# Kernel tuning notes

Hardware: AMD Instinct MI355X
Metric: run time of the kernel (lower is better)

The kernel has to match this reference:

```python
import jax, jax.numpy as jnp
import numpy as np

D_MODEL = 1024
N_HEADS = 16
HEAD_DIM = D_MODEL // N_HEADS


def setup_inputs() -> dict:
    key = jax.random.key(0)
    ks = jax.random.split(key, 6)
    B, S = 2, 2048
    scale = 1.0 / np.sqrt(D_MODEL)
    x = jax.random.normal(ks[0], (B, S, D_MODEL), dtype=jnp.float32)
    Wq = jax.random.normal(ks[1], (D_MODEL, D_MODEL), dtype=jnp.float32) * scale
    Wk = jax.random.normal(ks[2], (D_MODEL, D_MODEL), dtype=jnp.float32) * scale
    Wv = jax.random.normal(ks[3], (D_MODEL, D_MODEL), dtype=jnp.float32) * scale
    Wo = jax.random.normal(ks[4], (D_MODEL, D_MODEL), dtype=jnp.float32) * scale
    bo = jax.random.normal(ks[5], (D_MODEL,), dtype=jnp.float32) * 0.02
    return {"x": x, "Wq": Wq, "Wk": Wk, "Wv": Wv, "Wo": Wo, "bo": bo}


def reference(x, Wq, Wk, Wv, Wo, bo):
    B, S, _ = x.shape
    H, hd = N_HEADS, HEAD_DIM
    # qkv projections (no bias, qkv_bias=False)
    q = (x @ Wq).reshape(B, S, H, hd).transpose(0, 2, 1, 3)  # [B,H,S,hd]
    k = (x @ Wk).reshape(B, S, H, hd).transpose(0, 2, 1, 3)
    v = (x @ Wv).reshape(B, S, H, hd).transpose(0, 2, 1, 3)
    scores = jnp.einsum('bhqd,bhkd->bhqk', q, k)  # [B,H,S,S]
    causal = jnp.tril(jnp.ones((S, S), dtype=bool))  # True = keep
    scores = jnp.where(causal, scores, -jnp.inf)
    weights = jax.nn.softmax(scores / np.sqrt(hd), axis=-1)
    # dropout p=0.0 -> identity
    ctx = jnp.einsum('bhqk,bhkd->bhqd', weights, v)  # [B,H,S,hd]
    ctx = ctx.transpose(0, 2, 1, 3).reshape(B, S, H * hd)
    return ctx @ Wo + bo
```

## Files before the change

### kernel.cpp

```cpp
#include <hip/hip_runtime.h>
#include <hip/hip_bf16.h>
#include <stdint.h>

#define SEQ    2048
#define BATCH  2
#define DMODEL 1024
#define NHEADS 16
#define HDIM   64
#define MROWS  (BATCH*SEQ)

typedef __attribute__((ext_vector_type(8))) short bf16x8;
typedef __attribute__((ext_vector_type(4))) float f32x4;

__device__ inline void global_to_lds16(const void* g, void* l) {
  __builtin_amdgcn_global_load_lds(
      (const __attribute__((address_space(1))) uint32_t*)g,
      (__attribute__((address_space(3))) uint32_t*)l, 16, 0, 0);
}

__device__ inline unsigned short f2bf_bits(float f) {
  __hip_bfloat16 h = __float2bfloat16(f);
  return *(unsigned short*)&h;
}

__global__ void cvt_x(const float* __restrict__ x, __hip_bfloat16* __restrict__ xb) {
  int i = (blockIdx.x * 256 + threadIdx.x) * 4;
  float4 v = *(const float4*)(x + i);
  ushort4 o;
  o.x = f2bf_bits(v.x); o.y = f2bf_bits(v.y);
  o.z = f2bf_bits(v.z); o.w = f2bf_bits(v.w);
  *(ushort4*)(xb + i) = o;
}

__global__ void trans_w(const float* __restrict__ Wq, const float* __restrict__ Wk,
                        const float* __restrict__ Wv, const float* __restrict__ Wo,
                        __hip_bfloat16* __restrict__ Wqkv_t, __hip_bfloat16* __restrict__ Wo_t) {
  __shared__ float tile[32][33];
  int z = blockIdx.z;
  const float* W = (z == 0) ? Wq : (z == 1) ? Wk : (z == 2) ? Wv : Wo;
  __hip_bfloat16* dst = (z < 3) ? (Wqkv_t + (size_t)z * 1024 * 1024) : Wo_t;
  int k0 = blockIdx.x * 32, n0 = blockIdx.y * 32;
  int tx = threadIdx.x & 31, ty = threadIdx.x >> 5;
#pragma unroll
  for (int r = 0; r < 4; r++)
    tile[ty + r * 8][tx] = W[(size_t)(k0 + ty + r * 8) * 1024 + n0 + tx];
  __syncthreads();
#pragma unroll
  for (int r = 0; r < 4; r++)
    dst[(size_t)(n0 + ty + r * 8) * 1024 + k0 + tx] = __float2bfloat16(tile[tx][ty + r * 8]);
}

__global__ void trans_v(const __hip_bfloat16* __restrict__ QKV, __hip_bfloat16* __restrict__ Vt) {
  __shared__ __hip_bfloat16 tile[64][72];
  int bh = blockIdx.y;
  int b = bh >> 4, h = bh & 15;
  int s0 = blockIdx.x * 64;
  int t = threadIdx.x;
  int r = t >> 2, cg = (t & 3) * 16;
  const __hip_bfloat16* src = QKV + ((size_t)(b * SEQ + s0 + r)) * 3072 + 2048 + h * 64 + cg;
  *(uint4*)&tile[r][cg]     = *(const uint4*)src;
  *(uint4*)&tile[r][cg + 8] = *(const uint4*)(src + 8);
  __syncthreads();
  unsigned short tmp[16];
#pragma unroll
  for (int i = 0; i < 16; i++) tmp[i] = *(const unsigned short*)&tile[cg + i][r];
  __hip_bfloat16* dst = Vt + ((size_t)bh * 64 + r) * 2048 + s0 + cg;
  *(uint4*)dst       = *(const uint4*)&tmp[0];
  *(uint4*)(dst + 8) = *(const uint4*)&tmp[8];
}

template <int TN, bool OUT_BF16, int MINW>
__global__ __launch_bounds__(256, MINW)
void gemm_kernel(const __hip_bfloat16* __restrict__ A, const __hip_bfloat16* __restrict__ Bt,
                 void* __restrict__ C, const float* __restrict__ bias, int ldc) {
  __shared__ __hip_bfloat16 Asl[128 * 32];
  __shared__ __hip_bfloat16 Bsl[TN * 32];

  const int t = threadIdx.x;
  const int lane = t & 63;
  const int w = t >> 6;
  constexpr int MI = (TN == 128) ? 4 : 2;
  const int wrow = (TN == 128) ? (w >> 1) * 64 : w * 32;
  const int wcol = (TN == 128) ? (w & 1) * 64 : 0;
  const int m0 = blockIdx.y * 128;
  const int n0 = blockIdx.x * TN;

  f32x4 acc[MI][4];
#pragma unroll
  for (int i = 0; i < MI; i++)
#pragma unroll
    for (int j = 0; j < 4; j++) acc[i][j] = (f32x4){0.f, 0.f, 0.f, 0.f};

  const int rA0 = w * 16 + (lane >> 2);
  const int kof = (lane & 3) * 8;
  const int fm = lane & 15;
  const int fk = (lane >> 4) * 8;

  for (int k0 = 0; k0 < 1024; k0 += 32) {
#pragma unroll
    for (int i = 0; i < 2; i++) {
      int r = rA0 + i * 64;
      global_to_lds16(A + (size_t)(m0 + r) * 1024 + k0 + kof, (void*)(Asl + r * 32 + kof));
    }
#pragma unroll
    for (int i = 0; i < TN / 64; i++) {
      int r = rA0 + i * 64;
      global_to_lds16(Bt + (size_t)(n0 + r) * 1024 + k0 + kof, (void*)(Bsl + r * 32 + kof));
    }
    __syncthreads();
    bf16x8 af[MI], bfr[4];
#pragma unroll
    for (int mi = 0; mi < MI; mi++)
      af[mi] = *(const bf16x8*)(Asl + (wrow + mi * 16 + fm) * 32 + fk);
#pragma unroll
    for (int ni = 0; ni < 4; ni++)
      bfr[ni] = *(const bf16x8*)(Bsl + (wcol + ni * 16 + fm) * 32 + fk);
#pragma unroll
    for (int mi = 0; mi < MI; mi++)
#pragma unroll
      for (int ni = 0; ni < 4; ni++)
        acc[mi][ni] = __builtin_amdgcn_mfma_f32_16x16x32_bf16(af[mi], bfr[ni], acc[mi][ni], 0, 0, 0);
    __syncthreads();
  }

#pragma unroll
  for (int mi = 0; mi < MI; mi++) {
    int mb = m0 + wrow + mi * 16 + (lane >> 4) * 4;
#pragma unroll
    for (int ni = 0; ni < 4; ni++) {
      int n = n0 + wcol + ni * 16 + fm;
      float bv = OUT_BF16 ? 0.f : bias[n];
#pragma unroll
      for (int r = 0; r < 4; r++) {
        if (OUT_BF16)
          ((__hip_bfloat16*)C)[(size_t)(mb + r) * ldc + n] = __float2bfloat16(acc[mi][ni][r]);
        else
          ((float*)C)[(size_t)(mb + r) * ldc + n] = acc[mi][ni][r] + bv;
      }
    }
  }
}

__global__ __launch_bounds__(256, 2)
void attn_kernel(const __hip_bfloat16* __restrict__ QKV,
                 const __hip_bfloat16* __restrict__ Vt,
                 __hip_bfloat16* __restrict__ ctx) {
  __shared__ __hip_bfloat16 Klds[2][128 * 64];
  __shared__ __hip_bfloat16 Vlds[2][64 * 128];
  __shared__ __hip_bfloat16 Plds[64 * 72];

  const int t = threadIdx.x;
  const int lane = t & 63;
  const int w = t >> 6;
  const int jb = blockIdx.x;
  const int qtab[2] = { jb, 31 - jb };
  const int bh = blockIdx.y;
  const int b = bh >> 4, h = bh & 15;
  const int fm = lane & 15;
  const int g4 = lane >> 4;
  const int fk = g4 * 8;
  const size_t rowb = (size_t)b * SEQ;
  const float c = 0.18033688011112042f;

  const int krr = lane >> 3;
  const int kjc = (lane & 7) ^ krr;
  const int vrr = lane >> 4;
  const int vjc = (lane & 15) ^ ((w & 1) * 4 + vrr);

  bf16x8 qf[2][2];
#pragma unroll
  for (int hh = 0; hh < 2; hh++) {
    const __hip_bfloat16* qp = QKV + (rowb + qtab[hh] * 64 + w * 16 + fm) * 3072 + h * 64 + fk;
    bf16x8 r0 = *(const bf16x8*)qp;
    bf16x8 r1 = *(const bf16x8*)(qp + 32);
#pragma unroll
    for (int i = 0; i < 8; i++) {
      float f0 = __uint_as_float(((unsigned)(unsigned short)r0[i]) << 16) * c;
      float f1 = __uint_as_float(((unsigned)(unsigned short)r1[i]) << 16) * c;
      r0[i] = (short)f2bf_bits(f0);
      r1[i] = (short)f2bf_bits(f1);
    }
    qf[hh][0] = r0; qf[hh][1] = r1;
  }

  bf16x8 ones;
#pragma unroll
  for (int i = 0; i < 8; i++) ones[i] = (short)0x3F80;

  f32x4 acc[2][4];
  f32x4 lacc[2];
#pragma unroll
  for (int hh = 0; hh < 2; hh++) {
    lacc[hh] = (f32x4){0.f, 0.f, 0.f, 0.f};
#pragma unroll
    for (int d = 0; d < 4; d++) acc[hh][d] = (f32x4){0.f, 0.f, 0.f, 0.f};
  }

  auto stage = [&](int ktt2, int bufi) {
    const int kt0 = ktt2 * 128;
#pragma unroll
    for (int i = 0; i < 4; i++) {
      int seg = w + i * 4;
      int kr = seg * 8 + krr;
      global_to_lds16(QKV + (rowb + kt0 + kr) * 3072 + 1024 + h * 64 + kjc * 8,
                      (void*)(&Klds[bufi][0] + seg * 512 + lane * 8));
      int vr = seg * 4 + vrr;
      global_to_lds16(Vt + ((size_t)bh * 64 + vr) * 2048 + kt0 + vjc * 8,
                      (void*)(&Vlds[bufi][0] + seg * 512 + lane * 8));
    }
  };

  const int lastt = qtab[1] >> 1;
  stage(0, 0);
  for (int ktt2 = 0; ktt2 <= lastt; ++ktt2) {
    __syncthreads();
    if (ktt2 < lastt) stage(ktt2 + 1, (ktt2 + 1) & 1);
    const __hip_bfloat16* Kb = &Klds[ktt2 & 1][0];
    const __hip_bfloat16* Vb = &Vlds[ktt2 & 1][0];

#pragma unroll
    for (int sc = 0; sc < 2; sc++) {
      const int kts = ktt2 * 2 + sc;
#pragma unroll
      for (int hh = 0; hh < 2; hh++) {
        if (kts > qtab[hh]) continue;
        f32x4 s[4];
#pragma unroll
        for (int ns = 0; ns < 4; ns++) s[ns] = (f32x4){0.f, 0.f, 0.f, 0.f};
#pragma unroll
        for (int kk = 0; kk < 2; kk++) {
#pragma unroll
          for (int ns = 0; ns < 4; ns++) {
            int row = sc * 64 + ns * 16 + fm;
            bf16x8 kf = *(const bf16x8*)(Kb + row * 64 + (((kk * 4 + g4) ^ (fm & 7)) << 3));
            s[ns] = __builtin_amdgcn_mfma_f32_16x16x32_bf16(qf[hh][kk], kf, s[ns], 0, 0, 0);
          }
        }
        const bool diag = (kts == qtab[hh]);
#pragma unroll
        for (int ns = 0; ns < 4; ns++)
#pragma unroll
          for (int r = 0; r < 4; r++) {
            bool msk = diag && (ns * 16 + fm > w * 16 + g4 * 4 + r);
            float p = msk ? 0.f : __builtin_amdgcn_exp2f(s[ns][r]);
            Plds[(w * 16 + g4 * 4 + r) * 72 + ns * 16 + fm] = __float2bfloat16(p);
          }
#pragma unroll
        for (int kk = 0; kk < 2; kk++) {
          bf16x8 pa = *(const bf16x8*)(Plds + (w * 16 + fm) * 72 + kk * 32 + fk);
          lacc[hh] = __builtin_amdgcn_mfma_f32_16x16x32_bf16(pa, ones, lacc[hh], 0, 0, 0);
#pragma unroll
          for (int dd = 0; dd < 4; dd++) {
            int vslot = (sc * 8 + kk * 4 + g4) ^ (fm & 7);
            bf16x8 vf = *(const bf16x8*)(Vb + (dd * 16 + fm) * 128 + vslot * 8);
            acc[hh][dd] = __builtin_amdgcn_mfma_f32_16x16x32_bf16(pa, vf, acc[hh][dd], 0, 0, 0);
          }
        }
      }
    }
  }

#pragma unroll
  for (int hh = 0; hh < 2; hh++) {
    float rl[4];
#pragma unroll
    for (int r = 0; r < 4; r++) rl[r] = __builtin_amdgcn_rcpf(lacc[hh][r]);
#pragma unroll
    for (int dd = 0; dd < 4; dd++)
#pragma unroll
      for (int r = 0; r < 4; r++) {
        int q = qtab[hh] * 64 + w * 16 + g4 * 4 + r;
        ctx[(rowb + q) * 1024 + h * 64 + dd * 16 + fm] =
            __float2bfloat16(acc[hh][dd][r] * rl[r]);
      }
  }
}

extern "C" void kernel_launch(void* const* d_in, const int* in_sizes, int n_in,
                              void* d_out, int out_size, void* d_ws, size_t ws_size,
                              hipStream_t stream) {
  const float* x  = (const float*)d_in[0];
  const float* Wq = (const float*)d_in[1];
  const float* Wk = (const float*)d_in[2];
  const float* Wv = (const float*)d_in[3];
  const float* Wo = (const float*)d_in[4];
  const float* bo = (const float*)d_in[5];
  float* out = (float*)d_out;

  char* ws = (char*)d_ws;
  __hip_bfloat16* xb     = (__hip_bfloat16*)(ws);
  __hip_bfloat16* Wqkv_t = (__hip_bfloat16*)(ws + (8ull  << 20));
  __hip_bfloat16* Wo_t   = (__hip_bfloat16*)(ws + (14ull << 20));
  __hip_bfloat16* QKV    = (__hip_bfloat16*)(ws + (16ull << 20));
  __hip_bfloat16* ctxb   = (__hip_bfloat16*)(ws + (40ull << 20));
  __hip_bfloat16* Vt     = xb;

  cvt_x<<<dim3(MROWS * DMODEL / (256 * 4)), dim3(256), 0, stream>>>(x, xb);
  trans_w<<<dim3(32, 32, 4), dim3(256), 0, stream>>>(Wq, Wk, Wv, Wo, Wqkv_t, Wo_t);
  gemm_kernel<128, true, 3><<<dim3(24, 32), dim3(256), 0, stream>>>(xb, Wqkv_t, (void*)QKV, nullptr, 3072);
  trans_v<<<dim3(32, 32), dim3(256), 0, stream>>>(QKV, Vt);
  attn_kernel<<<dim3(16, 32), dim3(256), 0, stream>>>(QKV, Vt, ctxb);
  gemm_kernel<64, false, 2><<<dim3(16, 32), dim3(256), 0, stream>>>(ctxb, Wo_t, (void*)out, bo, 1024);
}
```

Baseline: 189.0 us.

## Shrink attention K/V tiles to 64 keys and transpose S to reuse K fragments

The attention kernel now stages 64-key K/V tiles instead of 128, which cuts LDS use and raises the launch-bounds occupancy target from 2 to 3 blocks per CU. S is computed transposed (K as A operand), so each loaded K fragment serves both query halves. P is written as packed 4-element swizzled stores into per-wave buffers. The cost is twice as many loop iterations and barriers, plus a tighter register budget under the higher occupancy hint, which may cause spills.

```diff
diff --git a/kernel.cpp b/kernel.cpp
--- a/kernel.cpp
+++ b/kernel.cpp
@@ -141,13 +141,13 @@
   }
 }
 
-__global__ __launch_bounds__(256, 2)
+__global__ __launch_bounds__(256, 3)
 void attn_kernel(const __hip_bfloat16* __restrict__ QKV,
                  const __hip_bfloat16* __restrict__ Vt,
                  __hip_bfloat16* __restrict__ ctx) {
-  __shared__ __hip_bfloat16 Klds[2][128 * 64];
-  __shared__ __hip_bfloat16 Vlds[2][64 * 128];
-  __shared__ __hip_bfloat16 Plds[64 * 72];
+  __shared__ __hip_bfloat16 Klds[2][64 * 64];
+  __shared__ __hip_bfloat16 Vlds[2][64 * 64];
+  __shared__ __hip_bfloat16 Plds[2][4][16 * 64];
 
   const int t = threadIdx.x;
   const int lane = t & 63;
@@ -164,8 +164,6 @@
 
   const int krr = lane >> 3;
   const int kjc = (lane & 7) ^ krr;
-  const int vrr = lane >> 4;
-  const int vjc = (lane & 15) ^ ((w & 1) * 4 + vrr);
 
   bf16x8 qf[2][2];
 #pragma unroll
@@ -196,68 +194,78 @@
     for (int d = 0; d < 4; d++) acc[hh][d] = (f32x4){0.f, 0.f, 0.f, 0.f};
   }
 
-  auto stage = [&](int ktt2, int bufi) {
-    const int kt0 = ktt2 * 128;
-#pragma unroll
-    for (int i = 0; i < 4; i++) {
+  auto stage = [&](int kts, int bufi) {
+    const int kt0 = kts * 64;
+#pragma unroll
+    for (int i = 0; i < 2; i++) {
       int seg = w + i * 4;
-      int kr = seg * 8 + krr;
-      global_to_lds16(QKV + (rowb + kt0 + kr) * 3072 + 1024 + h * 64 + kjc * 8,
+      int r = seg * 8 + krr;
+      global_to_lds16(QKV + (rowb + kt0 + r) * 3072 + 1024 + h * 64 + kjc * 8,
                       (void*)(&Klds[bufi][0] + seg * 512 + lane * 8));
-      int vr = seg * 4 + vrr;
-      global_to_lds16(Vt + ((size_t)bh * 64 + vr) * 2048 + kt0 + vjc * 8,
+      global_to_lds16(Vt + ((size_t)bh * 64 + r) * 2048 + kt0 + kjc * 8,
                       (void*)(&Vlds[bufi][0] + seg * 512 + lane * 8));
     }
   };
 
-  const int lastt = qtab[1] >> 1;
+  const int lastt = qtab[1];
   stage(0, 0);
-  for (int ktt2 = 0; ktt2 <= lastt; ++ktt2) {
+  for (int kts = 0; kts <= lastt; ++kts) {
     __syncthreads();
-    if (ktt2 < lastt) stage(ktt2 + 1, (ktt2 + 1) & 1);
-    const __hip_bfloat16* Kb = &Klds[ktt2 & 1][0];
-    const __hip_bfloat16* Vb = &Vlds[ktt2 & 1][0];
-
-#pragma unroll
-    for (int sc = 0; sc < 2; sc++) {
-      const int kts = ktt2 * 2 + sc;
-#pragma unroll
-      for (int hh = 0; hh < 2; hh++) {
-        if (kts > qtab[hh]) continue;
-        f32x4 s[4];
-#pragma unroll
-        for (int ns = 0; ns < 4; ns++) s[ns] = (f32x4){0.f, 0.f, 0.f, 0.f};
-#pragma unroll
-        for (int kk = 0; kk < 2; kk++) {
-#pragma unroll
-          for (int ns = 0; ns < 4; ns++) {
-            int row = sc * 64 + ns * 16 + fm;
-            bf16x8 kf = *(const bf16x8*)(Kb + row * 64 + (((kk * 4 + g4) ^ (fm & 7)) << 3));
-            s[ns] = __builtin_amdgcn_mfma_f32_16x16x32_bf16(qf[hh][kk], kf, s[ns], 0, 0, 0);
-          }
+    if (kts < lastt) stage(kts + 1, (kts + 1) & 1);
+    const __hip_bfloat16* Kb = &Klds[kts & 1][0];
+    const __hip_bfloat16* Vb = &Vlds[kts & 1][0];
+    const bool act0 = (kts <= qtab[0]);
+
+    f32x4 st1[4], st0[4];
+#pragma unroll
+    for (int ns = 0; ns < 4; ns++) {
+      st1[ns] = (f32x4){0.f, 0.f, 0.f, 0.f};
+      st0[ns] = (f32x4){0.f, 0.f, 0.f, 0.f};
+    }
+#pragma unroll
+    for (int kk = 0; kk < 2; kk++) {
+      bf16x8 kf[4];
+#pragma unroll
+      for (int ns = 0; ns < 4; ns++)
+        kf[ns] = *(const bf16x8*)(Kb + (ns * 16 + fm) * 64 + (((kk * 4 + g4) ^ (fm & 7)) << 3));
+#pragma unroll
+      for (int ns = 0; ns < 4; ns++)
+        st1[ns] = __builtin_amdgcn_mfma_f32_16x16x32_bf16(kf[ns], qf[1][kk], st1[ns], 0, 0, 0);
+      if (act0)
+#pragma unroll
+        for (int ns = 0; ns < 4; ns++)
+          st0[ns] = __builtin_amdgcn_mfma_f32_16x16x32_bf16(kf[ns], qf[0][kk], st0[ns], 0, 0, 0);
+    }
+
+    auto half = [&](const f32x4 (&st)[4], int hh) {
+      const bool diag = (kts == qtab[hh]);
+      __hip_bfloat16* Pw = &Plds[hh][w][0];
+#pragma unroll
+      for (int ns = 0; ns < 4; ns++) {
+        unsigned short u[4];
+#pragma unroll
+        for (int r = 0; r < 4; r++) {
+          int ktl = ns * 16 + g4 * 4 + r;
+          bool msk = diag && (ktl > w * 16 + fm);
+          float p = msk ? 0.f : __builtin_amdgcn_exp2f(st[ns][r]);
+          u[r] = f2bf_bits(p);
         }
-        const bool diag = (kts == qtab[hh]);
-#pragma unroll
-        for (int ns = 0; ns < 4; ns++)
-#pragma unroll
-          for (int r = 0; r < 4; r++) {
-            bool msk = diag && (ns * 16 + fm > w * 16 + g4 * 4 + r);
-            float p = msk ? 0.f : __builtin_amdgcn_exp2f(s[ns][r]);
-            Plds[(w * 16 + g4 * 4 + r) * 72 + ns * 16 + fm] = __float2bfloat16(p);
-          }
-#pragma unroll
-        for (int kk = 0; kk < 2; kk++) {
-          bf16x8 pa = *(const bf16x8*)(Plds + (w * 16 + fm) * 72 + kk * 32 + fk);
-          lacc[hh] = __builtin_amdgcn_mfma_f32_16x16x32_bf16(pa, ones, lacc[hh], 0, 0, 0);
-#pragma unroll
-          for (int dd = 0; dd < 4; dd++) {
-            int vslot = (sc * 8 + kk * 4 + g4) ^ (fm & 7);
-            bf16x8 vf = *(const bf16x8*)(Vb + (dd * 16 + fm) * 128 + vslot * 8);
-            acc[hh][dd] = __builtin_amdgcn_mfma_f32_16x16x32_bf16(pa, vf, acc[hh][dd], 0, 0, 0);
-          }
+        int c16 = (ns * 2 + (g4 >> 1)) ^ (fm & 7);
+        *(uint2*)(Pw + fm * 64 + c16 * 8 + (g4 & 1) * 4) = *(const uint2*)u;
+      }
+#pragma unroll
+      for (int kk = 0; kk < 2; kk++) {
+        bf16x8 pa = *(const bf16x8*)(Pw + fm * 64 + (((kk * 4 + g4) ^ (fm & 7)) << 3));
+        lacc[hh] = __builtin_amdgcn_mfma_f32_16x16x32_bf16(pa, ones, lacc[hh], 0, 0, 0);
+#pragma unroll
+        for (int dd = 0; dd < 4; dd++) {
+          bf16x8 vf = *(const bf16x8*)(Vb + (dd * 16 + fm) * 64 + (((kk * 4 + g4) ^ (fm & 7)) << 3));
+          acc[hh][dd] = __builtin_amdgcn_mfma_f32_16x16x32_bf16(pa, vf, acc[hh][dd], 0, 0, 0);
         }
       }
-    }
+    };
+    half(st1, 1);
+    if (act0) half(st0, 0);
   }
 
 #pragma unroll
```

Result: no change. 189.0 us (-0.0%).
